# Optimization experiments

Measured on AMD Instinct MI355X. Metric: run time of the kernel, lower is better.

Reference implementation:

```python
import jax, jax.numpy as jnp
import numpy as np

N = 100000      # nodes
E = 1000000     # edges
IN_V = 16       # in_vfeat
OUT_V = 16      # out_vfeat
IN_E = 4        # in_efeat
EPS = 1e-5      # BatchNorm eps
SLOPE = 0.01    # LeakyReLU negative slope


def setup_inputs() -> dict:
    key = jax.random.key(0)
    ks = jax.random.split(key, 9)
    v = jax.random.normal(ks[0], (N, IN_V), jnp.float32)
    e = jax.random.normal(ks[1], (E, IN_E), jnp.float32)
    edge_index = jax.random.randint(ks[2], (2, E), 0, N, jnp.int32)
    # edge_net: Linear(IN_E, IN_V*OUT_V)
    enet_w = jax.random.normal(ks[3], (IN_V * OUT_V, IN_E), jnp.float32) / np.sqrt(IN_E)
    enet_b = jax.random.normal(ks[4], (IN_V * OUT_V,), jnp.float32) * 0.01
    # NNConv root weight [IN_V, OUT_V] and bias [OUT_V]
    root = jax.random.normal(ks[5], (IN_V, OUT_V), jnp.float32) / np.sqrt(IN_V)
    bias = jax.random.normal(ks[6], (OUT_V,), jnp.float32) * 0.01
    # BatchNorm affine params
    gamma = jnp.ones((OUT_V,), jnp.float32) + 0.1 * jax.random.normal(ks[7], (OUT_V,), jnp.float32)
    beta = 0.1 * jax.random.normal(ks[8], (OUT_V,), jnp.float32)
    return {"v": v, "e": e, "edge_index": edge_index, "enet_w": enet_w,
            "enet_b": enet_b, "root": root, "bias": bias, "gamma": gamma, "beta": beta}


def reference(v, e, edge_index, enet_w, enet_b, root, bias, gamma, beta):
    n = v.shape[0]
    src, dst = edge_index[0], edge_index[1]
    # edge MLP -> per-edge [IN_V, OUT_V] weight matrix
    w = (e @ enet_w.T + enet_b).reshape(-1, IN_V, OUT_V)        # [E, in, out]
    # gather source features, per-edge matmul
    msg = jnp.einsum('ei,eio->eo', v[src], w)                   # [E, out]
    # scatter-mean to target nodes (degree-0 nodes -> 0, count clamped to 1)
    summed = jax.ops.segment_sum(msg, dst, num_segments=n)      # [N, out]
    cnt = jax.ops.segment_sum(jnp.ones((msg.shape[0],), v.dtype), dst, num_segments=n)
    out = summed / jnp.clip(cnt, 1.0)[:, None]
    # root transform + bias (NNConv)
    out = out + v @ root + bias
    # BatchNorm (training-mode batch stats) + LeakyReLU; dropout is Identity (dp=None)
    mu = out.mean(axis=0)
    var = out.var(axis=0)
    out = gamma * (out - mu) * jax.lax.rsqrt(var + EPS) + beta
    return jnp.where(out >= 0, out, SLOPE * out)
```

## Files before the change

kernel.cpp:

```cpp
#include <hip/hip_runtime.h>

#define N_NODES 100000
#define N_EDGES 1000000
#define EPS 1e-5f
#define SLOPE 0.01f
#define NBUCK 391
#define EPB 2560
#define NBINB 391
#define KSUB 8
#define SCAP 480
#define CCAP 3072


__global__ __launch_bounds__(256) void bin_kernel(
    const float* __restrict__ efeat,
    const int* __restrict__ edge_index,
    int* __restrict__ bcur,
    float4* __restrict__ Pb,
    unsigned short* __restrict__ dl)
{
    __shared__ int s_hist[NBUCK];
    __shared__ int s_base[NBUCK];

    const int tid = threadIdx.x;
    const int ksub = blockIdx.x & (KSUB - 1);
    const int e0 = blockIdx.x * EPB;
    const int e1 = min(e0 + EPB, N_EDGES);

    for (int i = tid; i < NBUCK; i += 256) s_hist[i] = 0;
    __syncthreads();
    for (int eid = e0 + tid; eid < e1; eid += 256) {
        int dst = edge_index[N_EDGES + eid];
        atomicAdd(&s_hist[dst >> 8], 1);
    }
    __syncthreads();

    for (int b = tid; b < NBUCK; b += 256) {
        int c = s_hist[b];
        s_base[b] = c ? atomicAdd(bcur + b * KSUB + ksub, c) : 0;
    }
    __syncthreads();
    for (int i = tid; i < NBUCK; i += 256) s_hist[i] = 0;
    __syncthreads();

    for (int eid = e0 + tid; eid < e1; eid += 256) {
        int src = edge_index[eid];
        int dst = edge_index[N_EDGES + eid];
        float4 ef = *(const float4*)(efeat + (size_t)eid * 4);
        int b = dst >> 8;
        int slot = s_base[b] + atomicAdd(&s_hist[b], 1);
        if (slot < SCAP) {
            size_t rec = ((size_t)b * KSUB + ksub) * SCAP + slot;
            Pb[2 * rec]     = ef;
            Pb[2 * rec + 1] = make_float4(__int_as_float(src), 0.f, 0.f, 0.f);
            dl[rec] = (unsigned short)(dst & 255);
        }
    }
}

__global__ __launch_bounds__(256) void gather_bucket_kernel(
    const float* __restrict__ v,
    const float4* __restrict__ Pb,
    const unsigned short* __restrict__ dl,
    const int* __restrict__ bcur,
    const float* __restrict__ enet_w,
    const float* __restrict__ enet_b,
    const float* __restrict__ root,
    const float* __restrict__ bias,
    float* __restrict__ out,
    float* __restrict__ stats)
{
    __shared__ unsigned short s_dl[CCAP];
    __shared__ unsigned short s_rec[CCAP];
    __shared__ unsigned short s_perm[CCAP];
    __shared__ int s_hist[256];
    __shared__ int s_sc[256];
    __shared__ int s_cur[256];
    __shared__ float s_part[4][32];

    const int b = blockIdx.x;
    const int tid = threadIdx.x;

    int ck[KSUB], off[KSUB];
    int cnt = 0;
    #pragma unroll
    for (int k = 0; k < KSUB; ++k) {
        int c = min(bcur[b * KSUB + k], SCAP);
        if (cnt + c > CCAP) c = CCAP - cnt;
        off[k] = cnt;
        ck[k] = c;
        cnt += c;
    }
    s_hist[tid] = 0;
    __syncthreads();
    #pragma unroll
    for (int k = 0; k < KSUB; ++k) {
        size_t segbase = ((size_t)b * KSUB + k) * SCAP;
        for (int i = tid; i < ck[k]; i += 256) {
            unsigned short d = dl[segbase + i];
            int pos = off[k] + i;
            s_dl[pos] = d;
            s_rec[pos] = (unsigned short)(k * SCAP + i);
            atomicAdd(&s_hist[d], 1);
        }
    }
    __syncthreads();

    int deg = s_hist[tid];
    s_sc[tid] = deg;
    __syncthreads();
    #pragma unroll
    for (int offs = 1; offs < 256; offs <<= 1) {
        int t = (tid >= offs) ? s_sc[tid - offs] : 0;
        __syncthreads();
        s_sc[tid] += t;
        __syncthreads();
    }
    int start = s_sc[tid] - deg;
    s_cur[tid] = start;
    __syncthreads();

    for (int i = tid; i < cnt; i += 256) {
        int slot = atomicAdd(&s_cur[s_dl[i]], 1);
        s_perm[slot] = s_rec[i];
    }
    __syncthreads();

    int n = b * 256 + tid;
    bool active = (n < N_NODES);

    float acc[80];
    #pragma unroll
    for (int i = 0; i < 80; ++i) acc[i] = 0.0f;

    const float4* pp = Pb + (size_t)2 * ((size_t)b * KSUB * SCAP);
    int j = 0;
    for (; j + 4 <= deg; j += 4) {
        int r0 = s_perm[start + j + 0];
        int r1 = s_perm[start + j + 1];
        int r2 = s_perm[start + j + 2];
        int r3 = s_perm[start + j + 3];
        float4 ef0 = pp[2*r0], sp0 = pp[2*r0+1];
        float4 ef1 = pp[2*r1], sp1 = pp[2*r1+1];
        float4 ef2 = pp[2*r2], sp2 = pp[2*r2+1];
        float4 ef3 = pp[2*r3], sp3 = pp[2*r3+1];
        int s0 = __float_as_int(sp0.x);
        int s1 = __float_as_int(sp1.x);
        int s2 = __float_as_int(sp2.x);
        int s3 = __float_as_int(sp3.x);
        const float4* vr0 = (const float4*)(v + (size_t)s0 * 16);
        const float4* vr1 = (const float4*)(v + (size_t)s1 * 16);
        const float4* vr2 = (const float4*)(v + (size_t)s2 * 16);
        const float4* vr3 = (const float4*)(v + (size_t)s3 * 16);
        #pragma unroll
        for (int i = 0; i < 4; ++i) {
            float4 a = vr0[i], bb = vr1[i], c = vr2[i], d = vr3[i];
            acc[     i*4+0] += (a.x + bb.x) + (c.x + d.x);
            acc[     i*4+1] += (a.y + bb.y) + (c.y + d.y);
            acc[     i*4+2] += (a.z + bb.z) + (c.z + d.z);
            acc[     i*4+3] += (a.w + bb.w) + (c.w + d.w);
            acc[16 + i*4+0] = fmaf(ef0.x, a.x, fmaf(ef1.x, bb.x,
                              fmaf(ef2.x, c.x, fmaf(ef3.x, d.x, acc[16 + i*4+0]))));
            acc[16 + i*4+1] = fmaf(ef0.x, a.y, fmaf(ef1.x, bb.y,
                              fmaf(ef2.x, c.y, fmaf(ef3.x, d.y, acc[16 + i*4+1]))));
            acc[16 + i*4+2] = fmaf(ef0.x, a.z, fmaf(ef1.x, bb.z,
                              fmaf(ef2.x, c.z, fmaf(ef3.x, d.z, acc[16 + i*4+2]))));
            acc[16 + i*4+3] = fmaf(ef0.x, a.w, fmaf(ef1.x, bb.w,
                              fmaf(ef2.x, c.w, fmaf(ef3.x, d.w, acc[16 + i*4+3]))));
            acc[32 + i*4+0] = fmaf(ef0.y, a.x, fmaf(ef1.y, bb.x,
                              fmaf(ef2.y, c.x, fmaf(ef3.y, d.x, acc[32 + i*4+0]))));
            acc[32 + i*4+1] = fmaf(ef0.y, a.y, fmaf(ef1.y, bb.y,
                              fmaf(ef2.y, c.y, fmaf(ef3.y, d.y, acc[32 + i*4+1]))));
            acc[32 + i*4+2] = fmaf(ef0.y, a.z, fmaf(ef1.y, bb.z,
                              fmaf(ef2.y, c.z, fmaf(ef3.y, d.z, acc[32 + i*4+2]))));
            acc[32 + i*4+3] = fmaf(ef0.y, a.w, fmaf(ef1.y, bb.w,
                              fmaf(ef2.y, c.w, fmaf(ef3.y, d.w, acc[32 + i*4+3]))));
            acc[48 + i*4+0] = fmaf(ef0.z, a.x, fmaf(ef1.z, bb.x,
                              fmaf(ef2.z, c.x, fmaf(ef3.z, d.x, acc[48 + i*4+0]))));
            acc[48 + i*4+1] = fmaf(ef0.z, a.y, fmaf(ef1.z, bb.y,
                              fmaf(ef2.z, c.y, fmaf(ef3.z, d.y, acc[48 + i*4+1]))));
            acc[48 + i*4+2] = fmaf(ef0.z, a.z, fmaf(ef1.z, bb.z,
                              fmaf(ef2.z, c.z, fmaf(ef3.z, d.z, acc[48 + i*4+2]))));
            acc[48 + i*4+3] = fmaf(ef0.z, a.w, fmaf(ef1.z, bb.w,
                              fmaf(ef2.z, c.w, fmaf(ef3.z, d.w, acc[48 + i*4+3]))));
            acc[64 + i*4+0] = fmaf(ef0.w, a.x, fmaf(ef1.w, bb.x,
                              fmaf(ef2.w, c.x, fmaf(ef3.w, d.x, acc[64 + i*4+0]))));
            acc[64 + i*4+1] = fmaf(ef0.w, a.y, fmaf(ef1.w, bb.y,
                              fmaf(ef2.w, c.y, fmaf(ef3.w, d.y, acc[64 + i*4+1]))));
            acc[64 + i*4+2] = fmaf(ef0.w, a.z, fmaf(ef1.w, bb.z,
                              fmaf(ef2.w, c.z, fmaf(ef3.w, d.z, acc[64 + i*4+2]))));
            acc[64 + i*4+3] = fmaf(ef0.w, a.w, fmaf(ef1.w, bb.w,
                              fmaf(ef2.w, c.w, fmaf(ef3.w, d.w, acc[64 + i*4+3]))));
        }
    }
    for (; j < deg; ++j) {
        int r0 = s_perm[start + j];
        float4 ef = pp[2*r0];
        float4 sp = pp[2*r0+1];
        int src = __float_as_int(sp.x);
        const float4* vr = (const float4*)(v + (size_t)src * 16);
        #pragma unroll
        for (int i = 0; i < 4; ++i) {
            float4 a = vr[i];
            acc[     i*4+0] += a.x;
            acc[     i*4+1] += a.y;
            acc[     i*4+2] += a.z;
            acc[     i*4+3] += a.w;
            acc[16 + i*4+0] = fmaf(ef.x, a.x, acc[16 + i*4+0]);
            acc[16 + i*4+1] = fmaf(ef.x, a.y, acc[16 + i*4+1]);
            acc[16 + i*4+2] = fmaf(ef.x, a.z, acc[16 + i*4+2]);
            acc[16 + i*4+3] = fmaf(ef.x, a.w, acc[16 + i*4+3]);
            acc[32 + i*4+0] = fmaf(ef.y, a.x, acc[32 + i*4+0]);
            acc[32 + i*4+1] = fmaf(ef.y, a.y, acc[32 + i*4+1]);
            acc[32 + i*4+2] = fmaf(ef.y, a.z, acc[32 + i*4+2]);
            acc[32 + i*4+3] = fmaf(ef.y, a.w, acc[32 + i*4+3]);
            acc[48 + i*4+0] = fmaf(ef.z, a.x, acc[48 + i*4+0]);
            acc[48 + i*4+1] = fmaf(ef.z, a.y, acc[48 + i*4+1]);
            acc[48 + i*4+2] = fmaf(ef.z, a.z, acc[48 + i*4+2]);
            acc[48 + i*4+3] = fmaf(ef.z, a.w, acc[48 + i*4+3]);
            acc[64 + i*4+0] = fmaf(ef.w, a.x, acc[64 + i*4+0]);
            acc[64 + i*4+1] = fmaf(ef.w, a.y, acc[64 + i*4+1]);
            acc[64 + i*4+2] = fmaf(ef.w, a.z, acc[64 + i*4+2]);
            acc[64 + i*4+3] = fmaf(ef.w, a.w, acc[64 + i*4+3]);
        }
    }

    float val[16];
    if (active) {
        float vn[16];
        #pragma unroll
        for (int i = 0; i < 4; ++i) {
            float4 tv = *(const float4*)(v + (size_t)n * 16 + i * 4);
            vn[4*i+0] = tv.x; vn[4*i+1] = tv.y;
            vn[4*i+2] = tv.z; vn[4*i+3] = tv.w;
        }
        float scale = 1.0f / fmaxf((float)deg, 1.0f);
        #pragma unroll
        for (int o = 0; o < 16; ++o) {
            float a = 0.0f;
            #pragma unroll
            for (int i = 0; i < 16; ++i) {
                a = fmaf(acc[i], enet_b[i * 16 + o], a);
                #pragma unroll
                for (int k = 0; k < 4; ++k)
                    a = fmaf(acc[16 + k * 16 + i],
                             enet_w[(i * 16 + o) * 4 + k], a);
            }
            a = fmaf(a, scale, bias[o]);
            #pragma unroll
            for (int i = 0; i < 16; ++i)
                a = fmaf(vn[i], root[i * 16 + o], a);
            val[o] = a;
        }
        #pragma unroll
        for (int i = 0; i < 4; ++i)
            *(float4*)(out + (size_t)n * 16 + i * 4) =
                make_float4(val[4*i+0], val[4*i+1], val[4*i+2], val[4*i+3]);
    } else {
        #pragma unroll
        for (int o = 0; o < 16; ++o) val[o] = 0.0f;
    }

    float ssum[16], ssq[16];
    #pragma unroll
    for (int o = 0; o < 16; ++o) {
        float a = val[o];
        float bsq = a * a;
        #pragma unroll
        for (int m = 1; m < 64; m <<= 1) {
            a += __shfl_xor(a, m, 64);
            bsq += __shfl_xor(bsq, m, 64);
        }
        ssum[o] = a; ssq[o] = bsq;
    }
    int wave = tid >> 6;
    int lane = tid & 63;
    if (lane == 0) {
        #pragma unroll
        for (int o = 0; o < 16; ++o) {
            s_part[wave][o]      = ssum[o];
            s_part[wave][16 + o] = ssq[o];
        }
    }
    __syncthreads();
    if (tid < 32) {
        float t = s_part[0][tid] + s_part[1][tid] +
                  s_part[2][tid] + s_part[3][tid];
        unsafeAtomicAdd(stats + tid, t);
    }
}

__global__ __launch_bounds__(256) void final_kernel(
    float* __restrict__ out,
    const float* __restrict__ stats,
    const float* __restrict__ gamma,
    const float* __restrict__ beta)
{
    int idx = blockIdx.x * 256 + threadIdx.x;
    if (idx >= N_NODES * 4) return;
    int o0 = (idx & 3) << 2;
    const float invN = 1.0f / (float)N_NODES;
    float4 x = *((const float4*)out + idx);
    float xs[4] = {x.x, x.y, x.z, x.w};
    float r[4];
    #pragma unroll
    for (int u = 0; u < 4; ++u) {
        int o = o0 + u;
        float mu = stats[o] * invN;
        float var = fmaxf(stats[16 + o] * invN - mu * mu, 0.0f);
        float y = fmaf(gamma[o] * (xs[u] - mu), rsqrtf(var + EPS), beta[o]);
        r[u] = (y >= 0.0f) ? y : SLOPE * y;
    }
    *((float4*)out + idx) = make_float4(r[0], r[1], r[2], r[3]);
}

extern "C" void kernel_launch(void* const* d_in, const int* in_sizes, int n_in,
                              void* d_out, int out_size, void* d_ws, size_t ws_size,
                              hipStream_t stream)
{
    const float* v = (const float*)d_in[0];
    const float* e = (const float*)d_in[1];
    const int* edge_index = (const int*)d_in[2];
    const float* enet_w = (const float*)d_in[3];
    const float* enet_b = (const float*)d_in[4];
    const float* root = (const float*)d_in[5];
    const float* bias = (const float*)d_in[6];
    const float* gamma = (const float*)d_in[7];
    const float* beta = (const float*)d_in[8];
    float* out = (float*)d_out;

    char* ws = (char*)d_ws;
    float4*         Pb    = (float4*)ws;  ws += (size_t)NBUCK * KSUB * SCAP * 32;
    unsigned short* dl    = (unsigned short*)ws;
                                          ws += (size_t)NBUCK * KSUB * SCAP * 2;
    int*            bcur  = (int*)ws;     ws += (size_t)NBUCK * KSUB * 4;
    float*          stats = (float*)ws;

    hipMemsetAsync(bcur, 0, (size_t)NBUCK * KSUB * 4 + 32 * 4, stream);

    bin_kernel<<<NBINB, 256, 0, stream>>>(e, edge_index, bcur, Pb, dl);
    gather_bucket_kernel<<<NBUCK, 256, 0, stream>>>(
        v, Pb, dl, bcur, enet_w, enet_b, root, bias, out, stats);
    final_kernel<<<(N_NODES * 4 + 255) / 256, 256, 0, stream>>>(
        out, stats, gamma, beta);
}
```

Measured before the change: 174.8 us.

## Split each node's aggregation across two threads with half the features each

The gather kernel now runs 512 threads per block, and two threads share each destination node. Each thread accumulates 8 of the 16 input features (40 accumulators instead of 80) and projects them through the edge-net weights. Partial messages are combined with a lane shuffle, and each thread then writes 8 output channels. The aim is to cut register pressure and double the thread parallelism across only 391 blocks, so memory latency is hidden better. The cost is that edge records are read twice per node and the unroll drops from 4 edges to 2.

```diff
diff --git a/kernel.cpp b/kernel.cpp
--- a/kernel.cpp
+++ b/kernel.cpp
@@ -58,7 +58,7 @@
     }
 }
 
-__global__ __launch_bounds__(256) void gather_bucket_kernel(
+__global__ __launch_bounds__(512, 4) void gather_bucket_kernel(
     const float* __restrict__ v,
     const float4* __restrict__ Pb,
     const unsigned short* __restrict__ dl,
@@ -76,7 +76,7 @@
     __shared__ int s_hist[256];
     __shared__ int s_sc[256];
     __shared__ int s_cur[256];
-    __shared__ float s_part[4][32];
+    __shared__ float s_part[8][32];
 
     const int b = blockIdx.x;
     const int tid = threadIdx.x;
@@ -91,12 +91,12 @@
         ck[k] = c;
         cnt += c;
     }
-    s_hist[tid] = 0;
+    if (tid < 256) s_hist[tid] = 0;
     __syncthreads();
     #pragma unroll
     for (int k = 0; k < KSUB; ++k) {
         size_t segbase = ((size_t)b * KSUB + k) * SCAP;
-        for (int i = tid; i < ck[k]; i += 256) {
+        for (int i = tid; i < ck[k]; i += 512) {
             unsigned short d = dl[segbase + i];
             int pos = off[k] + i;
             s_dl[pos] = d;
@@ -106,126 +106,111 @@
     }
     __syncthreads();
 
-    int deg = s_hist[tid];
-    s_sc[tid] = deg;
+    if (tid < 256) s_sc[tid] = s_hist[tid];
     __syncthreads();
     #pragma unroll
     for (int offs = 1; offs < 256; offs <<= 1) {
-        int t = (tid >= offs) ? s_sc[tid - offs] : 0;
+        int t = 0;
+        if (tid < 256 && tid >= offs) t = s_sc[tid - offs];
         __syncthreads();
-        s_sc[tid] += t;
+        if (tid < 256) s_sc[tid] += t;
         __syncthreads();
     }
-    int start = s_sc[tid] - deg;
-    s_cur[tid] = start;
-    __syncthreads();
-
-    for (int i = tid; i < cnt; i += 256) {
+    if (tid < 256) s_cur[tid] = s_sc[tid] - s_hist[tid];
+    __syncthreads();
+
+    for (int i = tid; i < cnt; i += 512) {
         int slot = atomicAdd(&s_cur[s_dl[i]], 1);
         s_perm[slot] = s_rec[i];
     }
     __syncthreads();
 
-    int n = b * 256 + tid;
-    bool active = (n < N_NODES);
-
-    float acc[80];
-    #pragma unroll
-    for (int i = 0; i < 80; ++i) acc[i] = 0.0f;
+    const int g = tid >> 1;
+    const int h = tid & 1;
+    const int n = b * 256 + g;
+    const bool active = (n < N_NODES);
+    const int deg = s_hist[g];
+    const int start = s_sc[g] - deg;
+
+    float acc[40];
+    #pragma unroll
+    for (int i = 0; i < 40; ++i) acc[i] = 0.0f;
 
     const float4* pp = Pb + (size_t)2 * ((size_t)b * KSUB * SCAP);
     int j = 0;
-    for (; j + 4 <= deg; j += 4) {
-        int r0 = s_perm[start + j + 0];
+    for (; j + 2 <= deg; j += 2) {
+        int r0 = s_perm[start + j];
         int r1 = s_perm[start + j + 1];
-        int r2 = s_perm[start + j + 2];
-        int r3 = s_perm[start + j + 3];
         float4 ef0 = pp[2*r0], sp0 = pp[2*r0+1];
         float4 ef1 = pp[2*r1], sp1 = pp[2*r1+1];
-        float4 ef2 = pp[2*r2], sp2 = pp[2*r2+1];
-        float4 ef3 = pp[2*r3], sp3 = pp[2*r3+1];
         int s0 = __float_as_int(sp0.x);
         int s1 = __float_as_int(sp1.x);
-        int s2 = __float_as_int(sp2.x);
-        int s3 = __float_as_int(sp3.x);
-        const float4* vr0 = (const float4*)(v + (size_t)s0 * 16);
-        const float4* vr1 = (const float4*)(v + (size_t)s1 * 16);
-        const float4* vr2 = (const float4*)(v + (size_t)s2 * 16);
-        const float4* vr3 = (const float4*)(v + (size_t)s3 * 16);
-        #pragma unroll
-        for (int i = 0; i < 4; ++i) {
-            float4 a = vr0[i], bb = vr1[i], c = vr2[i], d = vr3[i];
-            acc[     i*4+0] += (a.x + bb.x) + (c.x + d.x);
-            acc[     i*4+1] += (a.y + bb.y) + (c.y + d.y);
-            acc[     i*4+2] += (a.z + bb.z) + (c.z + d.z);
-            acc[     i*4+3] += (a.w + bb.w) + (c.w + d.w);
-            acc[16 + i*4+0] = fmaf(ef0.x, a.x, fmaf(ef1.x, bb.x,
-                              fmaf(ef2.x, c.x, fmaf(ef3.x, d.x, acc[16 + i*4+0]))));
-            acc[16 + i*4+1] = fmaf(ef0.x, a.y, fmaf(ef1.x, bb.y,
-                              fmaf(ef2.x, c.y, fmaf(ef3.x, d.y, acc[16 + i*4+1]))));
-            acc[16 + i*4+2] = fmaf(ef0.x, a.z, fmaf(ef1.x, bb.z,
-                              fmaf(ef2.x, c.z, fmaf(ef3.x, d.z, acc[16 + i*4+2]))));
-            acc[16 + i*4+3] = fmaf(ef0.x, a.w, fmaf(ef1.x, bb.w,
-                              fmaf(ef2.x, c.w, fmaf(ef3.x, d.w, acc[16 + i*4+3]))));
-            acc[32 + i*4+0] = fmaf(ef0.y, a.x, fmaf(ef1.y, bb.x,
-                              fmaf(ef2.y, c.x, fmaf(ef3.y, d.x, acc[32 + i*4+0]))));
-            acc[32 + i*4+1] = fmaf(ef0.y, a.y, fmaf(ef1.y, bb.y,
-                              fmaf(ef2.y, c.y, fmaf(ef3.y, d.y, acc[32 + i*4+1]))));
-            acc[32 + i*4+2] = fmaf(ef0.y, a.z, fmaf(ef1.y, bb.z,
-                              fmaf(ef2.y, c.z, fmaf(ef3.y, d.z, acc[32 + i*4+2]))));
-            acc[32 + i*4+3] = fmaf(ef0.y, a.w, fmaf(ef1.y, bb.w,
-                              fmaf(ef2.y, c.w, fmaf(ef3.y, d.w, acc[32 + i*4+3]))));
-            acc[48 + i*4+0] = fmaf(ef0.z, a.x, fmaf(ef1.z, bb.x,
-                              fmaf(ef2.z, c.x, fmaf(ef3.z, d.x, acc[48 + i*4+0]))));
-            acc[48 + i*4+1] = fmaf(ef0.z, a.y, fmaf(ef1.z, bb.y,
-                              fmaf(ef2.z, c.y, fmaf(ef3.z, d.y, acc[48 + i*4+1]))));
-            acc[48 + i*4+2] = fmaf(ef0.z, a.z, fmaf(ef1.z, bb.z,
-                              fmaf(ef2.z, c.z, fmaf(ef3.z, d.z, acc[48 + i*4+2]))));
-            acc[48 + i*4+3] = fmaf(ef0.z, a.w, fmaf(ef1.z, bb.w,
-                              fmaf(ef2.z, c.w, fmaf(ef3.z, d.w, acc[48 + i*4+3]))));
-            acc[64 + i*4+0] = fmaf(ef0.w, a.x, fmaf(ef1.w, bb.x,
-                              fmaf(ef2.w, c.x, fmaf(ef3.w, d.x, acc[64 + i*4+0]))));
-            acc[64 + i*4+1] = fmaf(ef0.w, a.y, fmaf(ef1.w, bb.y,
-                              fmaf(ef2.w, c.y, fmaf(ef3.w, d.y, acc[64 + i*4+1]))));
-            acc[64 + i*4+2] = fmaf(ef0.w, a.z, fmaf(ef1.w, bb.z,
-                              fmaf(ef2.w, c.z, fmaf(ef3.w, d.z, acc[64 + i*4+2]))));
-            acc[64 + i*4+3] = fmaf(ef0.w, a.w, fmaf(ef1.w, bb.w,
-                              fmaf(ef2.w, c.w, fmaf(ef3.w, d.w, acc[64 + i*4+3]))));
-        }
-    }
-    for (; j < deg; ++j) {
+        const float4* v0 = (const float4*)(v + (size_t)s0 * 16 + h * 8);
+        const float4* v1 = (const float4*)(v + (size_t)s1 * 16 + h * 8);
+        float4 a0 = v0[0], a1 = v0[1];
+        float4 b0 = v1[0], b1 = v1[1];
+        acc[ 0] += a0.x + b0.x;  acc[ 1] += a0.y + b0.y;
+        acc[ 2] += a0.z + b0.z;  acc[ 3] += a0.w + b0.w;
+        acc[ 4] += a1.x + b1.x;  acc[ 5] += a1.y + b1.y;
+        acc[ 6] += a1.z + b1.z;  acc[ 7] += a1.w + b1.w;
+        #define UPD(c, e0c, e1c) \
+            acc[8*(c)+0] = fmaf(e0c, a0.x, fmaf(e1c, b0.x, acc[8*(c)+0])); \
+            acc[8*(c)+1] = fmaf(e0c, a0.y, fmaf(e1c, b0.y, acc[8*(c)+1])); \
+            acc[8*(c)+2] = fmaf(e0c, a0.z, fmaf(e1c, b0.z, acc[8*(c)+2])); \
+            acc[8*(c)+3] = fmaf(e0c, a0.w, fmaf(e1c, b0.w, acc[8*(c)+3])); \
+            acc[8*(c)+4] = fmaf(e0c, a1.x, fmaf(e1c, b1.x, acc[8*(c)+4])); \
+            acc[8*(c)+5] = fmaf(e0c, a1.y, fmaf(e1c, b1.y, acc[8*(c)+5])); \
+            acc[8*(c)+6] = fmaf(e0c, a1.z, fmaf(e1c, b1.z, acc[8*(c)+6])); \
+            acc[8*(c)+7] = fmaf(e0c, a1.w, fmaf(e1c, b1.w, acc[8*(c)+7]));
+        UPD(1, ef0.x, ef1.x)
+        UPD(2, ef0.y, ef1.y)
+        UPD(3, ef0.z, ef1.z)
+        UPD(4, ef0.w, ef1.w)
+        #undef UPD
+    }
+    if (j < deg) {
         int r0 = s_perm[start + j];
-        float4 ef = pp[2*r0];
-        float4 sp = pp[2*r0+1];
-        int src = __float_as_int(sp.x);
-        const float4* vr = (const float4*)(v + (size_t)src * 16);
-        #pragma unroll
-        for (int i = 0; i < 4; ++i) {
-            float4 a = vr[i];
-            acc[     i*4+0] += a.x;
-            acc[     i*4+1] += a.y;
-            acc[     i*4+2] += a.z;
-            acc[     i*4+3] += a.w;
-            acc[16 + i*4+0] = fmaf(ef.x, a.x, acc[16 + i*4+0]);
-            acc[16 + i*4+1] = fmaf(ef.x, a.y, acc[16 + i*4+1]);
-            acc[16 + i*4+2] = fmaf(ef.x, a.z, acc[16 + i*4+2]);
-            acc[16 + i*4+3] = fmaf(ef.x, a.w, acc[16 + i*4+3]);
-            acc[32 + i*4+0] = fmaf(ef.y, a.x, acc[32 + i*4+0]);
-            acc[32 + i*4+1] = fmaf(ef.y, a.y, acc[32 + i*4+1]);
-            acc[32 + i*4+2] = fmaf(ef.y, a.z, acc[32 + i*4+2]);
-            acc[32 + i*4+3] = fmaf(ef.y, a.w, acc[32 + i*4+3]);
-            acc[48 + i*4+0] = fmaf(ef.z, a.x, acc[48 + i*4+0]);
-            acc[48 + i*4+1] = fmaf(ef.z, a.y, acc[48 + i*4+1]);
-            acc[48 + i*4+2] = fmaf(ef.z, a.z, acc[48 + i*4+2]);
-            acc[48 + i*4+3] = fmaf(ef.z, a.w, acc[48 + i*4+3]);
-            acc[64 + i*4+0] = fmaf(ef.w, a.x, acc[64 + i*4+0]);
-            acc[64 + i*4+1] = fmaf(ef.w, a.y, acc[64 + i*4+1]);
-            acc[64 + i*4+2] = fmaf(ef.w, a.z, acc[64 + i*4+2]);
-            acc[64 + i*4+3] = fmaf(ef.w, a.w, acc[64 + i*4+3]);
-        }
-    }
-
-    float val[16];
+        float4 ef0 = pp[2*r0], sp0 = pp[2*r0+1];
+        int s0 = __float_as_int(sp0.x);
+        const float4* v0 = (const float4*)(v + (size_t)s0 * 16 + h * 8);
+        float4 a0 = v0[0], a1 = v0[1];
+        acc[ 0] += a0.x;  acc[ 1] += a0.y;  acc[ 2] += a0.z;  acc[ 3] += a0.w;
+        acc[ 4] += a1.x;  acc[ 5] += a1.y;  acc[ 6] += a1.z;  acc[ 7] += a1.w;
+        #define UPD1(c, e0c) \
+            acc[8*(c)+0] = fmaf(e0c, a0.x, acc[8*(c)+0]); \
+            acc[8*(c)+1] = fmaf(e0c, a0.y, acc[8*(c)+1]); \
+            acc[8*(c)+2] = fmaf(e0c, a0.z, acc[8*(c)+2]); \
+            acc[8*(c)+3] = fmaf(e0c, a0.w, acc[8*(c)+3]); \
+            acc[8*(c)+4] = fmaf(e0c, a1.x, acc[8*(c)+4]); \
+            acc[8*(c)+5] = fmaf(e0c, a1.y, acc[8*(c)+5]); \
+            acc[8*(c)+6] = fmaf(e0c, a1.z, acc[8*(c)+6]); \
+            acc[8*(c)+7] = fmaf(e0c, a1.w, acc[8*(c)+7]);
+        UPD1(1, ef0.x)
+        UPD1(2, ef0.y)
+        UPD1(3, ef0.z)
+        UPD1(4, ef0.w)
+        #undef UPD1
+    }
+
+    float m[16];
+    #pragma unroll
+    for (int o = 0; o < 16; ++o) {
+        float a = 0.0f;
+        #pragma unroll
+        for (int il = 0; il < 8; ++il) {
+            int i = h * 8 + il;
+            a = fmaf(acc[il], enet_b[i * 16 + o], a);
+            #pragma unroll
+            for (int k = 0; k < 4; ++k)
+                a = fmaf(acc[(k + 1) * 8 + il],
+                         enet_w[(i * 16 + o) * 4 + k], a);
+        }
+        m[o] = a;
+    }
+    #pragma unroll
+    for (int o = 0; o < 16; ++o) m[o] += __shfl_xor(m[o], 1, 64);
+
+    float val8[8];
     if (active) {
         float vn[16];
         #pragma unroll
@@ -236,56 +221,49 @@
         }
         float scale = 1.0f / fmaxf((float)deg, 1.0f);
         #pragma unroll
-        for (int o = 0; o < 16; ++o) {
-            float a = 0.0f;
-            #pragma unroll
-            for (int i = 0; i < 16; ++i) {
-                a = fmaf(acc[i], enet_b[i * 16 + o], a);
-                #pragma unroll
-                for (int k = 0; k < 4; ++k)
-                    a = fmaf(acc[16 + k * 16 + i],
-                             enet_w[(i * 16 + o) * 4 + k], a);
-            }
-            a = fmaf(a, scale, bias[o]);
+        for (int u = 0; u < 8; ++u) {
+            int o = h * 8 + u;
+            float a = fmaf(m[o], scale, bias[o]);
             #pragma unroll
             for (int i = 0; i < 16; ++i)
                 a = fmaf(vn[i], root[i * 16 + o], a);
-            val[o] = a;
-        }
-        #pragma unroll
-        for (int i = 0; i < 4; ++i)
-            *(float4*)(out + (size_t)n * 16 + i * 4) =
-                make_float4(val[4*i+0], val[4*i+1], val[4*i+2], val[4*i+3]);
+            val8[u] = a;
+        }
+        *(float4*)(out + (size_t)n * 16 + h * 8)     =
+            make_float4(val8[0], val8[1], val8[2], val8[3]);
+        *(float4*)(out + (size_t)n * 16 + h * 8 + 4) =
+            make_float4(val8[4], val8[5], val8[6], val8[7]);
     } else {
         #pragma unroll
-        for (int o = 0; o < 16; ++o) val[o] = 0.0f;
-    }
-
-    float ssum[16], ssq[16];
-    #pragma unroll
-    for (int o = 0; o < 16; ++o) {
-        float a = val[o];
-        float bsq = a * a;
-        #pragma unroll
-        for (int m = 1; m < 64; m <<= 1) {
-            a += __shfl_xor(a, m, 64);
-            bsq += __shfl_xor(bsq, m, 64);
-        }
-        ssum[o] = a; ssq[o] = bsq;
+        for (int u = 0; u < 8; ++u) val8[u] = 0.0f;
+    }
+
+    float s1[8], s2[8];
+    #pragma unroll
+    for (int u = 0; u < 8; ++u) {
+        float a = val8[u];
+        float bq = a * a;
+        #pragma unroll
+        for (int mk = 2; mk < 64; mk <<= 1) {
+            a += __shfl_xor(a, mk, 64);
+            bq += __shfl_xor(bq, mk, 64);
+        }
+        s1[u] = a; s2[u] = bq;
     }
     int wave = tid >> 6;
     int lane = tid & 63;
-    if (lane == 0) {
-        #pragma unroll
-        for (int o = 0; o < 16; ++o) {
-            s_part[wave][o]      = ssum[o];
-            s_part[wave][16 + o] = ssq[o];
+    if (lane < 2) {
+        #pragma unroll
+        for (int u = 0; u < 8; ++u) {
+            s_part[wave][lane * 8 + u]      = s1[u];
+            s_part[wave][16 + lane * 8 + u] = s2[u];
         }
     }
     __syncthreads();
     if (tid < 32) {
-        float t = s_part[0][tid] + s_part[1][tid] +
-                  s_part[2][tid] + s_part[3][tid];
+        float t = 0.0f;
+        #pragma unroll
+        for (int w = 0; w < 8; ++w) t += s_part[w][tid];
         unsafeAtomicAdd(stats + tid, t);
     }
 }
@@ -339,7 +317,7 @@
     hipMemsetAsync(bcur, 0, (size_t)NBUCK * KSUB * 4 + 32 * 4, stream);
 
     bin_kernel<<<NBINB, 256, 0, stream>>>(e, edge_index, bcur, Pb, dl);
-    gather_bucket_kernel<<<NBUCK, 256, 0, stream>>>(
+    gather_bucket_kernel<<<NBUCK, 512, 0, stream>>>(
         v, Pb, dl, bcur, enet_w, enet_b, root, bias, out, stats);
     final_kernel<<<(N_NODES * 4 + 255) / 256, 256, 0, stream>>>(
         out, stats, gamma, beta);
```

Measured after the change: 195.6 us. 1.12x slower.
